# Optimization experiments

Hardware: AMD Instinct MI355X
Metric: run time of the kernel (lower is better)

Reference implementation:

```python
import jax, jax.numpy as jnp
import numpy as np

B, S, HID, USZ, PSZ, OUT = 128, 512, 768, 200, 200, 200
N_SENT = 16  # 16 sentences of 32 tokens; offsets row = [0,32,...,480,-1]


def setup_inputs() -> dict:
    key = jax.random.key(0)
    ks = jax.random.split(key, 8)
    H = jax.random.normal(ks[0], (B, S, HID), jnp.float32)
    u = jax.random.normal(ks[1], (B, USZ), jnp.float32)
    p = jax.random.normal(ks[2], (B, PSZ), jnp.float32)
    Wh = jax.random.normal(ks[3], (HID, OUT), jnp.float32) * 0.05
    Wu = jax.random.normal(ks[4], (USZ, OUT), jnp.float32) * 0.05
    Wp = jax.random.normal(ks[5], (PSZ, OUT), jnp.float32) * 0.05
    v = jax.random.normal(ks[6], (OUT,), jnp.float32) * 0.05
    b = jnp.zeros((OUT,), jnp.float32)  # torch buffer self.b = zeros
    # offsets: N_SENT sentence starts + trailing -1 sentinel -> [B, N_SENT+1]
    row = jnp.concatenate([jnp.arange(N_SENT, dtype=jnp.int32) * (S // N_SENT),
                           jnp.array([-1], jnp.int32)])
    sentence_offsets = jnp.tile(row[None, :], (B, 1))
    return {"H": H, "u": u, "p": p, "Wh": Wh, "Wu": Wu, "Wp": Wp,
            "v": v, "b": b, "sentence_offsets": sentence_offsets}


def reference(H, u, p, Wh, Wu, Wp, v, b, sentence_offsets):
    # Additive attention scores for every token: v . tanh(Wh H + Wu u + Wp p + b)
    Ht = jnp.einsum('bsh,ho->bso', H, Wh)                      # [B,S,OUT]
    ut = (u @ Wu)[:, None, :]                                  # [B,1,OUT]
    pt = (p @ Wp)[:, None, :]                                  # [B,1,OUT]
    scores = jnp.tanh(Ht + ut + pt + b) @ v                    # [B,S]

    Bsz, Sl, _ = H.shape
    beg = sentence_offsets[:, :-1]                             # [B,M]
    nxt = sentence_offsets[:, 1:]                              # [B,M]
    valid = beg != -1
    # faithful to torch: end = 512 if next==-1 else next-1 (off-by-one kept)
    end = jnp.where(nxt == -1, Sl, nxt - 1)
    t = jnp.arange(Sl)
    mask = valid[:, :, None] & (t[None, None, :] >= beg[:, :, None]) \
           & (t[None, None, :] < end[:, :, None])              # [B,M,S]

    neg_inf = jnp.float32(-jnp.inf)
    em = jnp.where(mask, scores[:, None, :], neg_inf)
    m = jnp.max(em, axis=-1, keepdims=True)
    w = jnp.exp(em - jnp.where(jnp.isfinite(m), m, 0.0)) * mask
    denom = jnp.sum(w, axis=-1, keepdims=True)
    alphas = w / jnp.where(denom > 0, denom, 1.0)              # ragged softmax
    # per-sentence weighted sum of H -> [B, M, HID] (invalid sentences = 0)
    return jnp.einsum('bms,bsh->bmh', alphas, H)
```

## Files before the change

### kernel.cpp

```cpp
#include <hip/hip_runtime.h>
#include <math.h>

#define Bn   128
#define Sn   512
#define HIDn 768
#define OUTn 200
#define MSEG 16
#define NPAD 224
#define NT   14
#define NTW  7
#define KIT  (HIDn / 32)

typedef __attribute__((ext_vector_type(8))) short short8;
typedef __attribute__((ext_vector_type(4))) float f32x4;

static __device__ inline unsigned short f2bf(float f) {
  union { float f; unsigned u; } v; v.f = f;
  unsigned r = v.u + 0x7FFFu + ((v.u >> 16) & 1u);
  return (unsigned short)(r >> 16);
}

static __device__ inline float fast_tanh(float x) {
  float t = fabsf(x);
  float e = __expf(-2.f * t);
  float r = (1.f - e) * __builtin_amdgcn_rcpf(1.f + e);
  return copysignf(r, x);
}

__global__ __launch_bounds__(256) void setup_kernel(
    const float* __restrict__ Wh, const float* __restrict__ v,
    unsigned short* __restrict__ WhF, float* __restrict__ vP) {
  int idx = blockIdx.x * 256 + threadIdx.x;
  if (blockIdx.x == 0 && threadIdx.x < NPAD)
    vP[threadIdx.x] = (threadIdx.x < OUTn) ? v[threadIdx.x] : 0.f;
  if (idx < NPAD * HIDn) {
    int n = idx / HIDn;
    int k = idx - n * HIDn;
    float val = (n < OUTn) ? Wh[(size_t)k * OUTn + n] : 0.f;
    size_t d = ((size_t)(k >> 5) * NT + (n >> 4)) * 512
             + ((k >> 3) & 3) * 128 + (n & 15) * 8 + (k & 7);
    WhF[d] = f2bf(val);
  }
}

__global__ __launch_bounds__(256) void bias_kernel(
    const float* __restrict__ u, const float* __restrict__ p,
    const float* __restrict__ Wu, const float* __restrict__ Wp,
    const float* __restrict__ bvec, float* __restrict__ biasP) {
  int b = blockIdx.x;
  __shared__ float ul[OUTn], pl[OUTn];
  int tid = threadIdx.x;
  if (tid < OUTn) { ul[tid] = u[b * OUTn + tid]; pl[tid] = p[b * OUTn + tid]; }
  __syncthreads();
  if (tid < NPAD) {
    float s0 = 0.f, s1 = 0.f;
    if (tid < OUTn) {
      s0 = bvec[tid];
      for (int k = 0; k < OUTn; k += 2) {
        s0 += ul[k] * Wu[k * OUTn + tid] + pl[k] * Wp[k * OUTn + tid];
        s1 += ul[k + 1] * Wu[(k + 1) * OUTn + tid] + pl[k + 1] * Wp[(k + 1) * OUTn + tid];
      }
    }
    biasP[(size_t)b * NPAD + tid] = s0 + s1;
  }
}

__global__ __launch_bounds__(256, 4) void fused_kernel(
    const float* __restrict__ H, const unsigned short* __restrict__ WhF,
    const float* __restrict__ biasP, const float* __restrict__ vP,
    const int* __restrict__ offs, float* __restrict__ out) {
  __shared__ float scp[2][32];
  __shared__ float o_l[4][HIDn];

  int tid = threadIdx.x, wave = tid >> 6, lane = tid & 63;
  int quad = lane >> 4, l16 = lane & 15;
  int mh = wave >> 1, nh = wave & 1;
  int bid = blockIdx.x;
  int b = bid >> 4, seg = bid & 15;
  int s0 = seg << 5;

  f32x4 acc[NTW];
#pragma unroll
  for (int j = 0; j < NTW; ++j) acc[j] = (f32x4){0.f, 0.f, 0.f, 0.f};

  const float* Abase = H + (size_t)(b * Sn + s0 + mh * 16 + l16) * HIDn + quad * 8;
  const short8* Bw = (const short8*)WhF + lane;

  float4 f[2][2];
  short8 bfr[2][NTW];
  f[0][0] = *(const float4*)Abase;
  f[0][1] = *(const float4*)(Abase + 4);
#pragma unroll
  for (int j = 0; j < NTW; ++j)
    bfr[0][j] = Bw[(nh * NTW + j) * 64];

#pragma unroll
  for (int it = 0; it < KIT; ++it) {
    int cur = it & 1;
    if (it + 1 < KIT) {
      const float* ap = Abase + (it + 1) * 32;
      f[1 - cur][0] = *(const float4*)ap;
      f[1 - cur][1] = *(const float4*)(ap + 4);
#pragma unroll
      for (int j = 0; j < NTW; ++j)
        bfr[1 - cur][j] = Bw[((it + 1) * NT + nh * NTW + j) * 64];
    }
    short8 a;
    a[0] = f2bf(f[cur][0].x); a[1] = f2bf(f[cur][0].y);
    a[2] = f2bf(f[cur][0].z); a[3] = f2bf(f[cur][0].w);
    a[4] = f2bf(f[cur][1].x); a[5] = f2bf(f[cur][1].y);
    a[6] = f2bf(f[cur][1].z); a[7] = f2bf(f[cur][1].w);
#pragma unroll
    for (int j = 0; j < NTW; ++j)
      acc[j] = __builtin_amdgcn_mfma_f32_16x16x32_bf16(a, bfr[cur][j], acc[j], 0, 0, 0);
  }

  {
    const float* bp = biasP + (size_t)b * NPAD + nh * (NTW * 16) + l16;
    const float* vp = vP + nh * (NTW * 16) + l16;
    float bv[NTW], vv[NTW];
#pragma unroll
    for (int j = 0; j < NTW; ++j) { bv[j] = bp[j * 16]; vv[j] = vp[j * 16]; }
#pragma unroll
    for (int r = 0; r < 4; ++r) {
      float s = 0.f;
#pragma unroll
      for (int j = 0; j < NTW; ++j)
        s += fast_tanh(acc[j][r] + bv[j]) * vv[j];
      s += __shfl_xor(s, 1); s += __shfl_xor(s, 2);
      s += __shfl_xor(s, 4); s += __shfl_xor(s, 8);
      if (l16 == 0) scp[nh][mh * 16 + quad * 4 + r] = s;
    }
  }
  __syncthreads();

  int beg = offs[b * (MSEG + 1) + seg];
  int nxt = offs[b * (MSEG + 1) + seg + 1];
  bool valid = (beg != -1);
  int end = (nxt == -1) ? Sn : nxt - 1;

  float x = -INFINITY;
  if (lane < 32) {
    int row = s0 + lane;
    if (valid && row >= beg && row < end)
      x = scp[0][lane] + scp[1][lane];
  }
  float mx = x;
  mx = fmaxf(mx, __shfl_xor(mx, 1));  mx = fmaxf(mx, __shfl_xor(mx, 2));
  mx = fmaxf(mx, __shfl_xor(mx, 4));  mx = fmaxf(mx, __shfl_xor(mx, 8));
  mx = fmaxf(mx, __shfl_xor(mx, 16)); mx = fmaxf(mx, __shfl_xor(mx, 32));
  float mm = (mx > -1e30f) ? mx : 0.f;
  float e = __expf(x - mm);
  float ls = e;
  ls += __shfl_xor(ls, 1);  ls += __shfl_xor(ls, 2);
  ls += __shfl_xor(ls, 4);  ls += __shfl_xor(ls, 8);
  ls += __shfl_xor(ls, 16); ls += __shfl_xor(ls, 32);
  float inv = (ls > 0.f) ? 1.f / ls : 0.f;
  float av = e * inv;

  float af[8];
#pragma unroll
  for (int i = 0; i < 8; ++i) af[i] = __shfl(av, wave * 8 + i);

  const float4* Hrow = (const float4*)(H + (size_t)(b * Sn + s0 + wave * 8) * HIDn);
  float4 o0 = {0,0,0,0}, o1 = {0,0,0,0}, o2 = {0,0,0,0};
#pragma unroll
  for (int i = 0; i < 8; ++i) {
    const float4* hp = Hrow + (size_t)i * (HIDn / 4);
    float4 h0 = hp[lane], h1 = hp[lane + 64], h2 = hp[lane + 128];
    float a = af[i];
    o0.x += a * h0.x; o0.y += a * h0.y; o0.z += a * h0.z; o0.w += a * h0.w;
    o1.x += a * h1.x; o1.y += a * h1.y; o1.z += a * h1.z; o1.w += a * h1.w;
    o2.x += a * h2.x; o2.y += a * h2.y; o2.z += a * h2.z; o2.w += a * h2.w;
  }
  {
    float4* ol = (float4*)o_l[wave];
    ol[lane] = o0; ol[lane + 64] = o1; ol[lane + 128] = o2;
  }
  __syncthreads();

  if (tid < 192) {
    const float4* p0 = (const float4*)o_l[0];
    const float4* p1 = (const float4*)o_l[1];
    const float4* p2 = (const float4*)o_l[2];
    const float4* p3 = (const float4*)o_l[3];
    float4 a0 = p0[tid], a1 = p1[tid], a2 = p2[tid], a3 = p3[tid];
    float4 s;
    s.x = a0.x + a1.x + a2.x + a3.x;
    s.y = a0.y + a1.y + a2.y + a3.y;
    s.z = a0.z + a1.z + a2.z + a3.z;
    s.w = a0.w + a1.w + a2.w + a3.w;
    ((float4*)(out + ((size_t)b * MSEG + seg) * HIDn))[tid] = s;
  }
}

extern "C" void kernel_launch(void* const* d_in, const int* in_sizes, int n_in,
                              void* d_out, int out_size, void* d_ws, size_t ws_size,
                              hipStream_t stream) {
  const float* H    = (const float*)d_in[0];
  const float* u    = (const float*)d_in[1];
  const float* p    = (const float*)d_in[2];
  const float* Wh   = (const float*)d_in[3];
  const float* Wu   = (const float*)d_in[4];
  const float* Wp   = (const float*)d_in[5];
  const float* v    = (const float*)d_in[6];
  const float* bvec = (const float*)d_in[7];
  const int*   offs = (const int*)d_in[8];
  float* out = (float*)d_out;

  float* biasP = (float*)d_ws;
  float* vP    = biasP + (size_t)Bn * NPAD;
  unsigned short* WhF = (unsigned short*)(vP + NPAD);

  setup_kernel<<<(NPAD * HIDn + 255) / 256, 256, 0, stream>>>(Wh, v, WhF, vP);
  bias_kernel<<<Bn, 256, 0, stream>>>(u, p, Wu, Wp, bvec, biasP);
  fused_kernel<<<(Bn * Sn) / 32, 256, 0, stream>>>(H, WhF, biasP, vP, offs, out);
}
```

Before: 403.6 us.

## Process two sentences per block with LDS-staged H tiles via direct global-to-LDS loads

```diff
diff --git a/kernel.cpp b/kernel.cpp
--- a/kernel.cpp
+++ b/kernel.cpp
@@ -9,10 +9,15 @@
 #define NPAD 224
 #define NT   14
 #define NTW  7
-#define KIT  (HIDn / 32)
+#define KIT  24
+#define ROWS 64
 
 typedef __attribute__((ext_vector_type(8))) short short8;
 typedef __attribute__((ext_vector_type(4))) float f32x4;
+
+#define GL2LDS(gp, lp) __builtin_amdgcn_global_load_lds(                  \
+    (const __attribute__((address_space(1))) void*)(gp),                  \
+    (__attribute__((address_space(3))) void*)(lp), 16, 0, 0)
 
 static __device__ inline unsigned short f2bf(float f) {
   union { float f; unsigned u; } v; v.f = f;
@@ -65,54 +70,72 @@
   }
 }
 
-__global__ __launch_bounds__(256, 4) void fused_kernel(
+__global__ __launch_bounds__(256) void fused_kernel(
     const float* __restrict__ H, const unsigned short* __restrict__ WhF,
     const float* __restrict__ biasP, const float* __restrict__ vP,
     const int* __restrict__ offs, float* __restrict__ out) {
-  __shared__ float scp[2][32];
+  __shared__ float As[2][ROWS * 32];
+  __shared__ float scp[2][ROWS];
   __shared__ float o_l[4][HIDn];
 
   int tid = threadIdx.x, wave = tid >> 6, lane = tid & 63;
   int quad = lane >> 4, l16 = lane & 15;
   int mh = wave >> 1, nh = wave & 1;
   int bid = blockIdx.x;
-  int b = bid >> 4, seg = bid & 15;
-  int s0 = seg << 5;
-
-  f32x4 acc[NTW];
-#pragma unroll
-  for (int j = 0; j < NTW; ++j) acc[j] = (f32x4){0.f, 0.f, 0.f, 0.f};
-
-  const float* Abase = H + (size_t)(b * Sn + s0 + mh * 16 + l16) * HIDn + quad * 8;
+  int b = bid >> 3;
+  int s0 = (bid & 7) << 6;
+  int seg0 = (bid & 7) << 1;
+
+  int rstage = wave * 16 + (lane >> 3);
+  int csrc   = (lane & 7) ^ ((lane >> 3) & 7);
+  const float* Hblk  = H + (size_t)(b * Sn + s0) * HIDn;
+  const float* gsrc0 = Hblk + (size_t)rstage * HIDn + csrc * 4;
+  const float* gsrc1 = Hblk + (size_t)(rstage + 8) * HIDn + csrc * 4;
+  int ldst0 = wave * 512;
+  int ldst1 = wave * 512 + 256;
+
+  GL2LDS(gsrc0, &As[0][ldst0]);
+  GL2LDS(gsrc1, &As[0][ldst1]);
+
+  f32x4 acc[2][NTW];
+#pragma unroll
+  for (int mt = 0; mt < 2; ++mt)
+#pragma unroll
+    for (int j = 0; j < NTW; ++j) acc[mt][j] = (f32x4){0.f, 0.f, 0.f, 0.f};
+
   const short8* Bw = (const short8*)WhF + lane;
-
-  float4 f[2][2];
-  short8 bfr[2][NTW];
-  f[0][0] = *(const float4*)Abase;
-  f[0][1] = *(const float4*)(Abase + 4);
-#pragma unroll
-  for (int j = 0; j < NTW; ++j)
-    bfr[0][j] = Bw[(nh * NTW + j) * 64];
-
-#pragma unroll
-  for (int it = 0; it < KIT; ++it) {
-    int cur = it & 1;
-    if (it + 1 < KIT) {
-      const float* ap = Abase + (it + 1) * 32;
-      f[1 - cur][0] = *(const float4*)ap;
-      f[1 - cur][1] = *(const float4*)(ap + 4);
-#pragma unroll
-      for (int j = 0; j < NTW; ++j)
-        bfr[1 - cur][j] = Bw[((it + 1) * NT + nh * NTW + j) * 64];
-    }
-    short8 a;
-    a[0] = f2bf(f[cur][0].x); a[1] = f2bf(f[cur][0].y);
-    a[2] = f2bf(f[cur][0].z); a[3] = f2bf(f[cur][0].w);
-    a[4] = f2bf(f[cur][1].x); a[5] = f2bf(f[cur][1].y);
-    a[6] = f2bf(f[cur][1].z); a[7] = f2bf(f[cur][1].w);
+  int sw = (l16 & 7) << 2;
+
+  __syncthreads();
+
+#pragma unroll
+  for (int kt = 0; kt < KIT; ++kt) {
+    int buf = kt & 1;
+    short8 bfr[NTW];
 #pragma unroll
     for (int j = 0; j < NTW; ++j)
-      acc[j] = __builtin_amdgcn_mfma_f32_16x16x32_bf16(a, bfr[cur][j], acc[j], 0, 0, 0);
+      bfr[j] = Bw[(kt * NT + nh * NTW + j) * 64];
+    if (kt + 1 < KIT) {
+      GL2LDS(gsrc0 + (kt + 1) * 32, &As[buf ^ 1][ldst0]);
+      GL2LDS(gsrc1 + (kt + 1) * 32, &As[buf ^ 1][ldst1]);
+    }
+    short8 a[2];
+#pragma unroll
+    for (int mt = 0; mt < 2; ++mt) {
+      const float* Ab = &As[buf][(mh * 32 + mt * 16 + l16) * 32];
+      float4 h0 = *(const float4*)(Ab + ((quad * 8)     ^ sw));
+      float4 h1 = *(const float4*)(Ab + ((quad * 8 + 4) ^ sw));
+      short8 t;
+      t[0] = f2bf(h0.x); t[1] = f2bf(h0.y); t[2] = f2bf(h0.z); t[3] = f2bf(h0.w);
+      t[4] = f2bf(h1.x); t[5] = f2bf(h1.y); t[6] = f2bf(h1.z); t[7] = f2bf(h1.w);
+      a[mt] = t;
+    }
+#pragma unroll
+    for (int j = 0; j < NTW; ++j) {
+      acc[0][j] = __builtin_amdgcn_mfma_f32_16x16x32_bf16(a[0], bfr[j], acc[0][j], 0, 0, 0);
+      acc[1][j] = __builtin_amdgcn_mfma_f32_16x16x32_bf16(a[1], bfr[j], acc[1][j], 0, 0, 0);
+    }
+    __syncthreads();
   }
 
   {
@@ -122,56 +145,52 @@
 #pragma unroll
     for (int j = 0; j < NTW; ++j) { bv[j] = bp[j * 16]; vv[j] = vp[j * 16]; }
 #pragma unroll
-    for (int r = 0; r < 4; ++r) {
-      float s = 0.f;
-#pragma unroll
-      for (int j = 0; j < NTW; ++j)
-        s += fast_tanh(acc[j][r] + bv[j]) * vv[j];
-      s += __shfl_xor(s, 1); s += __shfl_xor(s, 2);
-      s += __shfl_xor(s, 4); s += __shfl_xor(s, 8);
-      if (l16 == 0) scp[nh][mh * 16 + quad * 4 + r] = s;
-    }
-  }
-  __syncthreads();
-
+    for (int mt = 0; mt < 2; ++mt)
+#pragma unroll
+      for (int r = 0; r < 4; ++r) {
+        float s = 0.f;
+#pragma unroll
+        for (int j = 0; j < NTW; ++j)
+          s += fast_tanh(acc[mt][j][r] + bv[j]) * vv[j];
+        s += __shfl_xor(s, 1); s += __shfl_xor(s, 2);
+        s += __shfl_xor(s, 4); s += __shfl_xor(s, 8);
+        if (l16 == 0) scp[nh][mh * 32 + mt * 16 + quad * 4 + r] = s;
+      }
+  }
+  __syncthreads();
+
+  int g = lane >> 5;
+  int seg = seg0 + g;
   int beg = offs[b * (MSEG + 1) + seg];
   int nxt = offs[b * (MSEG + 1) + seg + 1];
   bool valid = (beg != -1);
   int end = (nxt == -1) ? Sn : nxt - 1;
-
-  float x = -INFINITY;
-  if (lane < 32) {
-    int row = s0 + lane;
-    if (valid && row >= beg && row < end)
-      x = scp[0][lane] + scp[1][lane];
-  }
+  int row = s0 + lane;
+  float x = (valid && row >= beg && row < end)
+              ? (scp[0][lane] + scp[1][lane]) : -INFINITY;
   float mx = x;
   mx = fmaxf(mx, __shfl_xor(mx, 1));  mx = fmaxf(mx, __shfl_xor(mx, 2));
   mx = fmaxf(mx, __shfl_xor(mx, 4));  mx = fmaxf(mx, __shfl_xor(mx, 8));
-  mx = fmaxf(mx, __shfl_xor(mx, 16)); mx = fmaxf(mx, __shfl_xor(mx, 32));
+  mx = fmaxf(mx, __shfl_xor(mx, 16));
   float mm = (mx > -1e30f) ? mx : 0.f;
   float e = __expf(x - mm);
   float ls = e;
   ls += __shfl_xor(ls, 1);  ls += __shfl_xor(ls, 2);
   ls += __shfl_xor(ls, 4);  ls += __shfl_xor(ls, 8);
-  ls += __shfl_xor(ls, 16); ls += __shfl_xor(ls, 32);
-  float inv = (ls > 0.f) ? 1.f / ls : 0.f;
-  float av = e * inv;
-
-  float af[8];
-#pragma unroll
-  for (int i = 0; i < 8; ++i) af[i] = __shfl(av, wave * 8 + i);
-
-  const float4* Hrow = (const float4*)(H + (size_t)(b * Sn + s0 + wave * 8) * HIDn);
+  ls += __shfl_xor(ls, 16);
+  float av = e * ((ls > 0.f) ? 1.f / ls : 0.f);
+
+  int sgi = wave >> 1, rh = wave & 1;
+  const float4* Hrow = (const float4*)(H + (size_t)(b * Sn + s0 + sgi * 32 + rh * 16) * HIDn);
   float4 o0 = {0,0,0,0}, o1 = {0,0,0,0}, o2 = {0,0,0,0};
-#pragma unroll
-  for (int i = 0; i < 8; ++i) {
+#pragma unroll 4
+  for (int i = 0; i < 16; ++i) {
+    float a4 = __shfl(av, sgi * 32 + rh * 16 + i);
     const float4* hp = Hrow + (size_t)i * (HIDn / 4);
     float4 h0 = hp[lane], h1 = hp[lane + 64], h2 = hp[lane + 128];
-    float a = af[i];
-    o0.x += a * h0.x; o0.y += a * h0.y; o0.z += a * h0.z; o0.w += a * h0.w;
-    o1.x += a * h1.x; o1.y += a * h1.y; o1.z += a * h1.z; o1.w += a * h1.w;
-    o2.x += a * h2.x; o2.y += a * h2.y; o2.z += a * h2.z; o2.w += a * h2.w;
+    o0.x += a4 * h0.x; o0.y += a4 * h0.y; o0.z += a4 * h0.z; o0.w += a4 * h0.w;
+    o1.x += a4 * h1.x; o1.y += a4 * h1.y; o1.z += a4 * h1.z; o1.w += a4 * h1.w;
+    o2.x += a4 * h2.x; o2.y += a4 * h2.y; o2.z += a4 * h2.z; o2.w += a4 * h2.w;
   }
   {
     float4* ol = (float4*)o_l[wave];
@@ -184,13 +203,13 @@
     const float4* p1 = (const float4*)o_l[1];
     const float4* p2 = (const float4*)o_l[2];
     const float4* p3 = (const float4*)o_l[3];
-    float4 a0 = p0[tid], a1 = p1[tid], a2 = p2[tid], a3 = p3[tid];
-    float4 s;
-    s.x = a0.x + a1.x + a2.x + a3.x;
-    s.y = a0.y + a1.y + a2.y + a3.y;
-    s.z = a0.z + a1.z + a2.z + a3.z;
-    s.w = a0.w + a1.w + a2.w + a3.w;
-    ((float4*)(out + ((size_t)b * MSEG + seg) * HIDn))[tid] = s;
+    float4 a0 = p0[tid], a1 = p1[tid];
+    float4 b0 = p2[tid], b1 = p3[tid];
+    float4 sA, sB;
+    sA.x = a0.x + a1.x; sA.y = a0.y + a1.y; sA.z = a0.z + a1.z; sA.w = a0.w + a1.w;
+    sB.x = b0.x + b1.x; sB.y = b0.y + b1.y; sB.z = b0.z + b1.z; sB.w = b0.w + b1.w;
+    ((float4*)(out + ((size_t)b * MSEG + seg0) * HIDn))[tid] = sA;
+    ((float4*)(out + ((size_t)b * MSEG + seg0 + 1) * HIDn))[tid] = sB;
   }
 }
 
@@ -214,5 +233,5 @@
 
   setup_kernel<<<(NPAD * HIDn + 255) / 256, 256, 0, stream>>>(Wh, v, WhF, vP);
   bias_kernel<<<Bn, 256, 0, stream>>>(u, p, Wu, Wp, bvec, biasP);
-  fused_kernel<<<(Bn * Sn) / 32, 256, 0, stream>>>(H, WhF, biasP, vP, offs, out);
-}
+  fused_kernel<<<(Bn * Sn) / ROWS, 256, 0, stream>>>(H, WhF, biasP, vP, offs, out);
+}
```

After: 375.8 us. 6.9% less time.

## Stage H tiles into LDS via async global_load_lds with double buffering

Applied to the files above, without the earlier changes.

```diff
diff --git a/kernel.cpp b/kernel.cpp
--- a/kernel.cpp
+++ b/kernel.cpp
@@ -9,10 +9,17 @@
 #define NPAD 224
 #define NT   14
 #define NTW  7
-#define KIT  (HIDn / 32)
+#define KIT  24
+#define ROWS 32
+#define PH   3
+#define KPP  8
 
 typedef __attribute__((ext_vector_type(8))) short short8;
 typedef __attribute__((ext_vector_type(4))) float f32x4;
+
+#define GL2LDS(gp, lp) __builtin_amdgcn_global_load_lds(                  \
+    (const __attribute__((address_space(1))) void*)(gp),                  \
+    (__attribute__((address_space(3))) void*)(lp), 16, 0, 0)
 
 static __device__ inline unsigned short f2bf(float f) {
   union { float f; unsigned u; } v; v.f = f;
@@ -65,54 +72,72 @@
   }
 }
 
-__global__ __launch_bounds__(256, 4) void fused_kernel(
+__global__ __launch_bounds__(256) void fused_kernel(
     const float* __restrict__ H, const unsigned short* __restrict__ WhF,
     const float* __restrict__ biasP, const float* __restrict__ vP,
     const int* __restrict__ offs, float* __restrict__ out) {
-  __shared__ float scp[2][32];
+  __shared__ float As[2][KPP * 1024];
+  __shared__ float scp[2][ROWS];
   __shared__ float o_l[4][HIDn];
 
   int tid = threadIdx.x, wave = tid >> 6, lane = tid & 63;
   int quad = lane >> 4, l16 = lane & 15;
   int mh = wave >> 1, nh = wave & 1;
   int bid = blockIdx.x;
-  int b = bid >> 4, seg = bid & 15;
+  int b = bid >> 4;
+  int seg = bid & 15;
   int s0 = seg << 5;
 
+  const float* Hblk = H + (size_t)(b * Sn + s0) * HIDn;
+
+  int rloc = lane >> 3;
+  int csrc = (lane & 7) ^ (rloc & 7);
+  const float* Hst = Hblk + (size_t)rloc * HIDn + csrc * 4;
+
+#define STAGE(ph, bf)                                                        \
+  {                                                                          \
+    _Pragma("unroll")                                                        \
+    for (int t = 0; t < 8; ++t) {                                            \
+      int i_ = wave * 8 + t;                                                 \
+      int ks_ = i_ >> 2, qt_ = i_ & 3;                                       \
+      GL2LDS(Hst + (size_t)(qt_ * 8) * HIDn + ((ph) * KPP + ks_) * 32,       \
+             &As[bf][ks_ * 1024 + qt_ * 256]);                               \
+    }                                                                        \
+  }
+
   f32x4 acc[NTW];
 #pragma unroll
   for (int j = 0; j < NTW; ++j) acc[j] = (f32x4){0.f, 0.f, 0.f, 0.f};
 
-  const float* Abase = H + (size_t)(b * Sn + s0 + mh * 16 + l16) * HIDn + quad * 8;
   const short8* Bw = (const short8*)WhF + lane;
-
-  float4 f[2][2];
-  short8 bfr[2][NTW];
-  f[0][0] = *(const float4*)Abase;
-  f[0][1] = *(const float4*)(Abase + 4);
-#pragma unroll
-  for (int j = 0; j < NTW; ++j)
-    bfr[0][j] = Bw[(nh * NTW + j) * 64];
-
-#pragma unroll
-  for (int it = 0; it < KIT; ++it) {
-    int cur = it & 1;
-    if (it + 1 < KIT) {
-      const float* ap = Abase + (it + 1) * 32;
-      f[1 - cur][0] = *(const float4*)ap;
-      f[1 - cur][1] = *(const float4*)(ap + 4);
+  int row = mh * 16 + l16;
+  int slot0 = (2 * quad) ^ (l16 & 7);
+
+  STAGE(0, 0);
+  __syncthreads();
+
+#pragma unroll
+  for (int ph = 0; ph < PH; ++ph) {
+    int bf = ph & 1;
+#pragma unroll
+    for (int ks = 0; ks < KPP; ++ks) {
+      int kk = ph * KPP + ks;
+      short8 bfr[NTW];
 #pragma unroll
       for (int j = 0; j < NTW; ++j)
-        bfr[1 - cur][j] = Bw[((it + 1) * NT + nh * NTW + j) * 64];
+        bfr[j] = Bw[(kk * NT + nh * NTW + j) * 64];
+      if (ks == 2 && ph + 1 < PH) STAGE(ph + 1, bf ^ 1);
+      const float* Ab = &As[bf][ks * 1024 + row * 32];
+      float4 h0 = *(const float4*)(Ab + slot0 * 4);
+      float4 h1 = *(const float4*)(Ab + (slot0 ^ 1) * 4);
+      short8 a;
+      a[0] = f2bf(h0.x); a[1] = f2bf(h0.y); a[2] = f2bf(h0.z); a[3] = f2bf(h0.w);
+      a[4] = f2bf(h1.x); a[5] = f2bf(h1.y); a[6] = f2bf(h1.z); a[7] = f2bf(h1.w);
+#pragma unroll
+      for (int j = 0; j < NTW; ++j)
+        acc[j] = __builtin_amdgcn_mfma_f32_16x16x32_bf16(a, bfr[j], acc[j], 0, 0, 0);
     }
-    short8 a;
-    a[0] = f2bf(f[cur][0].x); a[1] = f2bf(f[cur][0].y);
-    a[2] = f2bf(f[cur][0].z); a[3] = f2bf(f[cur][0].w);
-    a[4] = f2bf(f[cur][1].x); a[5] = f2bf(f[cur][1].y);
-    a[6] = f2bf(f[cur][1].z); a[7] = f2bf(f[cur][1].w);
-#pragma unroll
-    for (int j = 0; j < NTW; ++j)
-      acc[j] = __builtin_amdgcn_mfma_f32_16x16x32_bf16(a, bfr[cur][j], acc[j], 0, 0, 0);
+    __syncthreads();
   }
 
   {
@@ -141,8 +166,8 @@
 
   float x = -INFINITY;
   if (lane < 32) {
-    int row = s0 + lane;
-    if (valid && row >= beg && row < end)
+    int rw = s0 + lane;
+    if (valid && rw >= beg && rw < end)
       x = scp[0][lane] + scp[1][lane];
   }
   float mx = x;
@@ -214,5 +239,5 @@
 
   setup_kernel<<<(NPAD * HIDn + 255) / 256, 256, 0, stream>>>(Wh, v, WhF, vP);
   bias_kernel<<<Bn, 256, 0, stream>>>(u, p, Wu, Wp, bvec, biasP);
-  fused_kernel<<<(Bn * Sn) / 32, 256, 0, stream>>>(H, WhF, biasP, vP, offs, out);
-}
+  fused_kernel<<<(Bn * Sn) / ROWS, 256, 0, stream>>>(H, WhF, biasP, vP, offs, out);
+}
```

After: 375.6 us. -6.9%, faster.
